# Performance work log

Measured on AMD Instinct MI355X. Metric: run time of the kernel, lower is better.

## Reference

```python
import jax, jax.numpy as jnp
import numpy as np

IN_DIM = 768
ATT_DIM = 512
N_HEADS = 8
HEAD_DIM = ATT_DIM // N_HEADS


def setup_inputs() -> dict:
    key = jax.random.key(0)
    k1, k2, k3 = jax.random.split(key, 3)
    X = jax.random.normal(k1, (4, 2048, IN_DIM), dtype=jnp.float32)
    # qkv linear (no bias): weight [3*att_dim, in_dim], torch convention y = x W^T
    W_qkv = jax.random.normal(k2, (3 * ATT_DIM, IN_DIM), dtype=jnp.float32) * (1.0 / np.sqrt(IN_DIM))
    W_out = jax.random.normal(k3, (IN_DIM, ATT_DIM), dtype=jnp.float32) * (1.0 / np.sqrt(ATT_DIM))
    b_out = jnp.zeros((IN_DIM,), dtype=jnp.float32)
    return {"X": X, "W_qkv": W_qkv, "W_out": W_out, "b_out": b_out}


def reference(X, W_qkv, W_out, b_out):
    b, n, _ = X.shape
    QKV = jnp.einsum('bnf,cf->bnc', X, W_qkv)  # [b, n, 3*att_dim]
    # rearrange 'b n (p h d) -> p b h n d'
    QKV = QKV.reshape(b, n, 3, N_HEADS, HEAD_DIM).transpose(2, 0, 3, 1, 4)
    Q, K, V = QKV[0], QKV[1], QKV[2]  # each [b, h, n, d]
    scores = jnp.einsum('bhid,bhjd->bhij', Q, K) / np.sqrt(HEAD_DIM)
    A = jax.nn.softmax(scores, axis=-1)  # dropout p=0 -> identity
    Y = jnp.einsum('bhij,bhjd->bhid', A, V)
    Y = Y.transpose(0, 2, 1, 3).reshape(b, n, ATT_DIM)  # 'b h n d -> b n (h d)'
    return jnp.einsum('bna,oa->bno', Y, W_out) + b_out
```

## Files before the change

### kernel.cpp

```cpp
#include <hip/hip_runtime.h>

typedef __bf16 bf16;
typedef unsigned int u32;
typedef __attribute__((ext_vector_type(8))) __bf16 bf16x8;
typedef __attribute__((ext_vector_type(4))) __bf16 bf16x4;
typedef __attribute__((ext_vector_type(4))) float floatx4;
typedef __attribute__((ext_vector_type(16))) float floatx16;
typedef __attribute__((ext_vector_type(4))) int int4v;

#define IN_DIM  768
#define ATT_DIM 512
#define NH      8
#define HD      64
#define BATCH   4
#define SEQ     2048
#define M_TOT   (BATCH*SEQ)
#define QKV_N   (3*ATT_DIM)

#define QSCALE 0.18033688011112042f

__device__ __forceinline__ void cp16(void* lds, const void* g) {
    __builtin_amdgcn_global_load_lds((const __attribute__((address_space(1))) u32*)g,
                                     (__attribute__((address_space(3))) u32*)lds, 16, 0, 0);
}
__device__ __forceinline__ const bf16* swz(const bf16* b, int row, int chunk) {
    return b + row * 64 + (((chunk) ^ (row & 7)) << 3);
}
__device__ __forceinline__ const bf16* swz128(const bf16* b, int row, int chunk) {
    return b + row * 128 + (((chunk) ^ (row & 15)) << 3);
}

__device__ __forceinline__ int cvtpk_bf16(float lo, float hi) {
    int r;
    asm("v_cvt_pk_bf16_f32 %0, %1, %2" : "=v"(r) : "v"(lo), "v"(hi));
    return r;
}
__device__ __forceinline__ void plswap(int& a, int& b) {
    asm("v_permlane32_swap_b32 %0, %1" : "+v"(a), "+v"(b));
}

#define N8_X  (M_TOT * IN_DIM / 8)
#define N8_WQ (QKV_N * IN_DIM / 8)
#define N8_WO (IN_DIM * ATT_DIM / 8)
#define N8_ALL (N8_X + N8_WQ + N8_WO)

__global__ __launch_bounds__(256) void cvt_all(const float* __restrict__ X,
                                               const float* __restrict__ Wq,
                                               const float* __restrict__ Wo,
                                               bf16* __restrict__ Xb,
                                               bf16* __restrict__ Wqb,
                                               bf16* __restrict__ Wob) {
    int i = blockIdx.x * 256 + threadIdx.x;
    const float* s; bf16* d; int off;
    if (i < N8_X)            { s = X;  d = Xb;  off = i; }
    else if (i < N8_X+N8_WQ) { s = Wq; d = Wqb; off = i - N8_X; }
    else                     { s = Wo; d = Wob; off = i - N8_X - N8_WQ; }
    const float4 a = ((const float4*)s)[2*off];
    const float4 b = ((const float4*)s)[2*off+1];
    bf16x8 o = {(bf16)a.x,(bf16)a.y,(bf16)a.z,(bf16)a.w,
                (bf16)b.x,(bf16)b.y,(bf16)b.z,(bf16)b.w};
    ((bf16x8*)d)[off] = o;
}

__global__ __launch_bounds__(256) void qkv_gemm(const bf16* __restrict__ Xb,
                                                const bf16* __restrict__ Wb,
                                                bf16* __restrict__ Q,
                                                bf16* __restrict__ Kv,
                                                bf16* __restrict__ VT) {
    __shared__ __align__(16) char smraw[34816];
    bf16* As = (bf16*)smraw;
    bf16* Bs = (bf16*)(smraw + 16384);

    const int tid  = threadIdx.x;
    const int bm0  = blockIdx.y * 128;
    const int bn0  = blockIdx.x * 128;
    const int wave = tid >> 6, lane = tid & 63;
    const int quad = lane >> 4, l15 = lane & 15;
    const int wm = (wave >> 1) * 64, wn = (wave & 1) * 64;
    const int r8 = lane >> 3, cc = (lane & 7) ^ r8;

    const bf16* ag = Xb + (size_t)(bm0 + wave * 32 + r8) * IN_DIM + cc * 8;
    const bf16* bg = Wb + (size_t)(bn0 + wave * 32 + r8) * IN_DIM + cc * 8;

    floatx4 acc[4][4];
#pragma unroll
    for (int i = 0; i < 4; ++i)
#pragma unroll
        for (int j = 0; j < 4; ++j) acc[i][j] = (floatx4){0.f, 0.f, 0.f, 0.f};

    for (int kt = 0; kt < IN_DIM / 64; ++kt) {
        __syncthreads();
#pragma unroll
        for (int it = 0; it < 4; ++it) {
            cp16(&As[(wave * 32 + it * 8) * 64], ag + it * (8 * IN_DIM) + kt * 64);
            cp16(&Bs[(wave * 32 + it * 8) * 64], bg + it * (8 * IN_DIM) + kt * 64);
        }
        __syncthreads();

        bf16x8 af[2][4], bfr[2][4];
#pragma unroll
        for (int kh = 0; kh < 2; ++kh)
#pragma unroll
            for (int i = 0; i < 4; ++i) {
                af[kh][i]  = *(const bf16x8*)swz(As, wm + i * 16 + l15, kh * 4 + quad);
                bfr[kh][i] = *(const bf16x8*)swz(Bs, wn + i * 16 + l15, kh * 4 + quad);
            }
#pragma unroll
        for (int kh = 0; kh < 2; ++kh)
#pragma unroll
            for (int i = 0; i < 4; ++i)
#pragma unroll
                for (int j = 0; j < 4; ++j)
                    acc[i][j] = __builtin_amdgcn_mfma_f32_16x16x32_bf16(af[kh][i], bfr[kh][j], acc[i][j], 0, 0, 0);
    }

    const int b = bm0 >> 11, nbase = bm0 & 2047;

    if (bn0 < 1024) {
#pragma unroll
        for (int i = 0; i < 4; ++i)
#pragma unroll
            for (int j = 0; j < 4; ++j)
#pragma unroll
                for (int r = 0; r < 4; ++r) {
                    const int row = bm0 + wm + i * 16 + quad * 4 + r;
                    const int col = bn0 + wn + j * 16 + l15;
                    const float v = acc[i][j][r];
                    const int rem = col & 511;
                    const int h = rem >> 6, d = rem & 63;
                    const int n = row & 2047;
                    const size_t idx = (((size_t)((row >> 11) * NH + h)) * SEQ + n) * HD + d;
                    if (col < 512) Q[idx]  = (bf16)(v * QSCALE);
                    else           Kv[idx] = (bf16)v;
                }
    } else {
        __syncthreads();
        bf16 (*Ts)[136] = (bf16(*)[136])smraw;
#pragma unroll
        for (int i = 0; i < 4; ++i)
#pragma unroll
            for (int j = 0; j < 4; ++j) {
                bf16x4 pk = {(bf16)acc[i][j][0], (bf16)acc[i][j][1],
                             (bf16)acc[i][j][2], (bf16)acc[i][j][3]};
                *(bf16x4*)&Ts[wn + j * 16 + l15][wm + i * 16 + quad * 4] = pk;
            }
        __syncthreads();
        const int cb = bn0 - 1024;
#pragma unroll
        for (int t2 = 0; t2 < 8; ++t2) {
            const int id = tid + t2 * 256;
            const int c = id >> 4, nc = (id & 15) * 8;
            const int col = cb + c;
            const int h = col >> 6, d = col & 63;
            *(bf16x8*)&VT[(((size_t)(b * NH + h)) * HD + d) * SEQ + nbase + nc] =
                *(const bf16x8*)&Ts[c][nc];
        }
    }
}

__global__ __launch_bounds__(256, 4) void attn(const bf16* __restrict__ Q,
                                               const bf16* __restrict__ K,
                                               const bf16* __restrict__ VT,
                                               bf16* __restrict__ Y) {
    __shared__ bf16 Ks[2][64 * 64];
    __shared__ bf16 VTs[2][64 * 64];

    const int tid  = threadIdx.x;
    const int wave = tid >> 6, lane = tid & 63;
    const int l31  = lane & 31, hi = lane >> 5;
    const int bh = blockIdx.x;
    const int q0 = blockIdx.y * 128;
    const bf16* Qg = Q  + (size_t)bh * SEQ * HD;
    const bf16* Kg = K  + (size_t)bh * SEQ * HD;
    const bf16* Vg = VT + (size_t)bh * HD * SEQ;

    bf16x8 aq[4];
    {
        const bf16* qrow = Qg + (size_t)(q0 + wave * 32 + l31) * HD;
#pragma unroll
        for (int c = 0; c < 4; ++c)
            aq[c] = *(const bf16x8*)(qrow + c * 16 + hi * 8);
    }

    const int r8 = lane >> 3, cc8 = (lane & 7) ^ r8;
    const bf16* kgw = Kg + (size_t)(wave * 16 + r8) * HD + cc8 * 8;
    const bf16* vgw = Vg + (size_t)(wave * 16 + r8) * SEQ + cc8 * 8;

    float l = 0.f;
    floatx16 o[2];
#pragma unroll
    for (int i = 0; i < 16; ++i) { o[0][i] = 0.f; o[1][i] = 0.f; }

#pragma unroll
    for (int it = 0; it < 2; ++it) {
        cp16(&Ks[0][(wave * 16 + it * 8) * 64], kgw + (size_t)(it * 8) * HD);
        cp16(&VTs[0][(wave * 16 + it * 8) * 64], vgw + (size_t)(it * 8) * SEQ);
    }

    for (int kt = 0; kt < SEQ / 64; ++kt) {
        const int cur = kt & 1;
        __syncthreads();
        if (kt < SEQ / 64 - 1) {
#pragma unroll
            for (int it = 0; it < 2; ++it) {
                cp16(&Ks[cur ^ 1][(wave * 16 + it * 8) * 64],
                     kgw + (size_t)((kt + 1) * 64 + it * 8) * HD);
                cp16(&VTs[cur ^ 1][(wave * 16 + it * 8) * 64],
                     vgw + (size_t)(it * 8) * SEQ + (kt + 1) * 64);
            }
        }

#pragma unroll
        for (int kb = 0; kb < 2; ++kb) {
            const int krow = kb * 32 + l31;
            floatx16 s;
#pragma unroll
            for (int i = 0; i < 16; ++i) s[i] = 0.f;
#pragma unroll
            for (int c = 0; c < 4; ++c) {
                const bf16x8 kf = *(const bf16x8*)swz(Ks[cur], krow, c * 2 + hi);
                s = __builtin_amdgcn_mfma_f32_32x32x16_bf16(kf, aq[c], s, 0, 0, 0);
            }
            float p[16];
#pragma unroll
            for (int i = 0; i < 16; ++i) p[i] = __builtin_amdgcn_exp2f(s[i]);
            {
                const float t0 = (p[0] + p[1]) + (p[2] + p[3]);
                const float t1 = (p[4] + p[5]) + (p[6] + p[7]);
                const float t2 = (p[8] + p[9]) + (p[10] + p[11]);
                const float t3 = (p[12] + p[13]) + (p[14] + p[15]);
                l += (t0 + t1) + (t2 + t3);
            }
            int w[8];
#pragma unroll
            for (int i = 0; i < 8; ++i) w[i] = cvtpk_bf16(p[2 * i], p[2 * i + 1]);
            plswap(w[0], w[2]); plswap(w[1], w[3]);
            plswap(w[4], w[6]); plswap(w[5], w[7]);
            const int4v f0i = {w[0], w[1], w[2], w[3]};
            const int4v f1i = {w[4], w[5], w[6], w[7]};
            const bf16x8 f0 = __builtin_bit_cast(bf16x8, f0i);
            const bf16x8 f1 = __builtin_bit_cast(bf16x8, f1i);
#pragma unroll
            for (int db = 0; db < 2; ++db) {
                const int vrow = db * 32 + l31;
                const bf16x8 v0 = *(const bf16x8*)swz(VTs[cur], vrow, kb * 4 + hi);
                const bf16x8 v1 = *(const bf16x8*)swz(VTs[cur], vrow, kb * 4 + 2 + hi);
                o[db] = __builtin_amdgcn_mfma_f32_32x32x16_bf16(f0, v0, o[db], 0, 0, 0);
                o[db] = __builtin_amdgcn_mfma_f32_32x32x16_bf16(f1, v1, o[db], 0, 0, 0);
            }
        }
    }

    l += __shfl_xor(l, 32, 64);
    const float inv = 1.0f / l;
    const int b = bh >> 3, h = bh & 7;
#pragma unroll
    for (int reg = 0; reg < 16; ++reg) {
        const int qr = (reg & 3) + 8 * (reg >> 2) + 4 * hi;
        const float li = __int_as_float(
            __builtin_amdgcn_ds_bpermute(qr << 2, __float_as_int(inv)));
        const int n = q0 + wave * 32 + qr;
        bf16* yrow = Y + ((size_t)(b * SEQ + n)) * ATT_DIM + h * HD + l31;
        yrow[0]  = (bf16)(o[0][reg] * li);
        yrow[32] = (bf16)(o[1][reg] * li);
    }
}

__global__ __launch_bounds__(256) void out_gemm(const bf16* __restrict__ Yb,
                                                const bf16* __restrict__ Wb,
                                                const float* __restrict__ bias,
                                                float* __restrict__ out) {
    __shared__ __align__(16) bf16 As[128 * 64];
    __shared__ __align__(16) bf16 Bs[128 * 64];

    const int tid  = threadIdx.x;
    const int bm0  = blockIdx.y * 128;
    const int bn0  = blockIdx.x * 128;
    const int wave = tid >> 6, lane = tid & 63;
    const int quad = lane >> 4, l15 = lane & 15;
    const int wm = (wave >> 1) * 64, wn = (wave & 1) * 64;
    const int r8 = lane >> 3, cc = (lane & 7) ^ r8;

    const bf16* ag = Yb + (size_t)(bm0 + wave * 32 + r8) * ATT_DIM + cc * 8;
    const bf16* bg = Wb + (size_t)(bn0 + wave * 32 + r8) * ATT_DIM + cc * 8;

    floatx4 acc[4][4];
#pragma unroll
    for (int i = 0; i < 4; ++i)
#pragma unroll
        for (int j = 0; j < 4; ++j) acc[i][j] = (floatx4){0.f, 0.f, 0.f, 0.f};

    for (int kt = 0; kt < ATT_DIM / 64; ++kt) {
        __syncthreads();
#pragma unroll
        for (int it = 0; it < 4; ++it) {
            cp16(&As[(wave * 32 + it * 8) * 64], ag + it * (8 * ATT_DIM) + kt * 64);
            cp16(&Bs[(wave * 32 + it * 8) * 64], bg + it * (8 * ATT_DIM) + kt * 64);
        }
        __syncthreads();

        bf16x8 af[2][4], bfr[2][4];
#pragma unroll
        for (int kh = 0; kh < 2; ++kh)
#pragma unroll
            for (int i = 0; i < 4; ++i) {
                af[kh][i]  = *(const bf16x8*)swz(As, wm + i * 16 + l15, kh * 4 + quad);
                bfr[kh][i] = *(const bf16x8*)swz(Bs, wn + i * 16 + l15, kh * 4 + quad);
            }
#pragma unroll
        for (int kh = 0; kh < 2; ++kh)
#pragma unroll
            for (int i = 0; i < 4; ++i)
#pragma unroll
                for (int j = 0; j < 4; ++j)
                    acc[i][j] = __builtin_amdgcn_mfma_f32_16x16x32_bf16(af[kh][i], bfr[kh][j], acc[i][j], 0, 0, 0);
    }

#pragma unroll
    for (int i = 0; i < 4; ++i)
#pragma unroll
        for (int j = 0; j < 4; ++j)
#pragma unroll
            for (int r = 0; r < 4; ++r) {
                const int row = bm0 + wm + i * 16 + quad * 4 + r;
                const int col = bn0 + wn + j * 16 + l15;
                out[(size_t)row * IN_DIM + col] = acc[i][j][r] + bias[col];
            }
}

extern "C" void kernel_launch(void* const* d_in, const int* in_sizes, int n_in,
                              void* d_out, int out_size, void* d_ws, size_t ws_size,
                              hipStream_t stream) {
    const float* X    = (const float*)d_in[0];
    const float* Wqkv = (const float*)d_in[1];
    const float* Wout = (const float*)d_in[2];
    const float* bout = (const float*)d_in[3];
    float* out = (float*)d_out;

    char* ws = (char*)d_ws;
    size_t off = 0;
    bf16* Xb  = (bf16*)(ws + off); off += (size_t)M_TOT * IN_DIM * 2;
    bf16* Wqb = (bf16*)(ws + off); off += (size_t)QKV_N * IN_DIM * 2;
    bf16* Wob = (bf16*)(ws + off); off += (size_t)IN_DIM * ATT_DIM * 2;
    const size_t T = (size_t)BATCH * NH * SEQ * HD * 2;
    bf16* Q  = (bf16*)(ws + off); off += T;
    bf16* K  = (bf16*)(ws + off); off += T;
    bf16* VT = (bf16*)(ws + off); off += T;
    bf16* Y  = (bf16*)(ws + off); off += T;

    cvt_all<<<N8_ALL / 256, 256, 0, stream>>>(X, Wqkv, Wout, Xb, Wqb, Wob);
    qkv_gemm<<<dim3(QKV_N / 128, M_TOT / 128), 256, 0, stream>>>(Xb, Wqb, Q, K, VT);
    attn<<<dim3(BATCH * NH, SEQ / 128), 256, 0, stream>>>(Q, K, VT, Y);
    out_gemm<<<dim3(IN_DIM / 128, M_TOT / 128), 256, 0, stream>>>(Y, Wob, bout, out);
}
```

Before: 162.7 us.

## Process two query groups per wave in attention and pre-permute K/VT for split LDS reads

Each attention wave now handles 64 query rows (two 32-row groups) instead of 32, so one set of K and V fragments read from LDS feeds twice as many MFMAs. Blocks shrink to 128 threads with launch_bounds(128,1). The QKV GEMM epilogue also stores K and VT with 8-byte halves swapped on alternating rows, and the attention kernel reads them back as two 8-byte LDS loads in swapped order, presumably to avoid bank conflicts. The cost is doubled accumulator register pressure and fewer waves per block, and the occupancy hint of 1 may limit latency hiding.

```diff
diff --git a/kernel.cpp b/kernel.cpp
--- a/kernel.cpp
+++ b/kernel.cpp
@@ -26,8 +26,12 @@
 __device__ __forceinline__ const bf16* swz(const bf16* b, int row, int chunk) {
     return b + row * 64 + (((chunk) ^ (row & 7)) << 3);
 }
-__device__ __forceinline__ const bf16* swz128(const bf16* b, int row, int chunk) {
-    return b + row * 128 + (((chunk) ^ (row & 15)) << 3);
+__device__ __forceinline__ bf16x8 ld_swz8(const bf16* tile, int row, int chunk) {
+    const char* base = (const char*)(tile + row * 64) + (((chunk ^ (row & 7)) << 4));
+    const int off = row & 8;
+    const bf16x4 h0 = *(const bf16x4*)(base + off);
+    const bf16x4 h1 = *(const bf16x4*)(base + (off ^ 8));
+    return (bf16x8){h0[0], h0[1], h0[2], h0[3], h1[0], h1[1], h1[2], h1[3]};
 }
 
 __device__ __forceinline__ int cvtpk_bf16(float lo, float hi) {
@@ -130,8 +134,8 @@
                     const int h = rem >> 6, d = rem & 63;
                     const int n = row & 2047;
                     const size_t idx = (((size_t)((row >> 11) * NH + h)) * SEQ + n) * HD + d;
-                    if (col < 512) Q[idx]  = (bf16)(v * QSCALE);
-                    else           Kv[idx] = (bf16)v;
+                    if (col < 512) Q[idx] = (bf16)(v * QSCALE);
+                    else           Kv[idx ^ (size_t)((n >> 1) & 4)] = (bf16)v;
                 }
     } else {
         __syncthreads();
@@ -152,13 +156,15 @@
             const int c = id >> 4, nc = (id & 15) * 8;
             const int col = cb + c;
             const int h = col >> 6, d = col & 63;
-            *(bf16x8*)&VT[(((size_t)(b * NH + h)) * HD + d) * SEQ + nbase + nc] =
-                *(const bf16x8*)&Ts[c][nc];
-        }
-    }
-}
-
-__global__ __launch_bounds__(256, 4) void attn(const bf16* __restrict__ Q,
+            bf16x8 val = *(const bf16x8*)&Ts[c][nc];
+            if (d & 8)
+                val = __builtin_shufflevector(val, val, 4, 5, 6, 7, 0, 1, 2, 3);
+            *(bf16x8*)&VT[(((size_t)(b * NH + h)) * HD + d) * SEQ + nbase + nc] = val;
+        }
+    }
+}
+
+__global__ __launch_bounds__(128, 1) void attn(const bf16* __restrict__ Q,
                                                const bf16* __restrict__ K,
                                                const bf16* __restrict__ VT,
                                                bf16* __restrict__ Y) {
@@ -174,27 +180,30 @@
     const bf16* Kg = K  + (size_t)bh * SEQ * HD;
     const bf16* Vg = VT + (size_t)bh * HD * SEQ;
 
-    bf16x8 aq[4];
-    {
-        const bf16* qrow = Qg + (size_t)(q0 + wave * 32 + l31) * HD;
+    bf16x8 aq[2][4];
+#pragma unroll
+    for (int g = 0; g < 2; ++g) {
+        const bf16* qrow = Qg + (size_t)(q0 + wave * 64 + g * 32 + l31) * HD;
 #pragma unroll
         for (int c = 0; c < 4; ++c)
-            aq[c] = *(const bf16x8*)(qrow + c * 16 + hi * 8);
+            aq[g][c] = *(const bf16x8*)(qrow + c * 16 + hi * 8);
     }
 
     const int r8 = lane >> 3, cc8 = (lane & 7) ^ r8;
-    const bf16* kgw = Kg + (size_t)(wave * 16 + r8) * HD + cc8 * 8;
-    const bf16* vgw = Vg + (size_t)(wave * 16 + r8) * SEQ + cc8 * 8;
-
-    float l = 0.f;
-    floatx16 o[2];
-#pragma unroll
-    for (int i = 0; i < 16; ++i) { o[0][i] = 0.f; o[1][i] = 0.f; }
-
-#pragma unroll
-    for (int it = 0; it < 2; ++it) {
-        cp16(&Ks[0][(wave * 16 + it * 8) * 64], kgw + (size_t)(it * 8) * HD);
-        cp16(&VTs[0][(wave * 16 + it * 8) * 64], vgw + (size_t)(it * 8) * SEQ);
+    const bf16* kgw = Kg + (size_t)(wave * 32 + r8) * HD + cc8 * 8;
+    const bf16* vgw = Vg + (size_t)(wave * 32 + r8) * SEQ + cc8 * 8;
+
+    float l[2] = {0.f, 0.f};
+    floatx16 o[2][2];
+#pragma unroll
+    for (int g = 0; g < 2; ++g)
+#pragma unroll
+        for (int i = 0; i < 16; ++i) { o[g][0][i] = 0.f; o[g][1][i] = 0.f; }
+
+#pragma unroll
+    for (int it = 0; it < 4; ++it) {
+        cp16(&Ks[0][(wave * 32 + it * 8) * 64], kgw + (size_t)(it * 8) * HD);
+        cp16(&VTs[0][(wave * 32 + it * 8) * 64], vgw + (size_t)(it * 8) * SEQ);
     }
 
     for (int kt = 0; kt < SEQ / 64; ++kt) {
@@ -202,10 +211,10 @@
         __syncthreads();
         if (kt < SEQ / 64 - 1) {
 #pragma unroll
-            for (int it = 0; it < 2; ++it) {
-                cp16(&Ks[cur ^ 1][(wave * 16 + it * 8) * 64],
+            for (int it = 0; it < 4; ++it) {
+                cp16(&Ks[cur ^ 1][(wave * 32 + it * 8) * 64],
                      kgw + (size_t)((kt + 1) * 64 + it * 8) * HD);
-                cp16(&VTs[cur ^ 1][(wave * 16 + it * 8) * 64],
+                cp16(&VTs[cur ^ 1][(wave * 32 + it * 8) * 64],
                      vgw + (size_t)(it * 8) * SEQ + (kt + 1) * 64);
             }
         }
@@ -213,56 +222,68 @@
 #pragma unroll
         for (int kb = 0; kb < 2; ++kb) {
             const int krow = kb * 32 + l31;
-            floatx16 s;
-#pragma unroll
-            for (int i = 0; i < 16; ++i) s[i] = 0.f;
-#pragma unroll
-            for (int c = 0; c < 4; ++c) {
-                const bf16x8 kf = *(const bf16x8*)swz(Ks[cur], krow, c * 2 + hi);
-                s = __builtin_amdgcn_mfma_f32_32x32x16_bf16(kf, aq[c], s, 0, 0, 0);
-            }
-            float p[16];
-#pragma unroll
-            for (int i = 0; i < 16; ++i) p[i] = __builtin_amdgcn_exp2f(s[i]);
-            {
-                const float t0 = (p[0] + p[1]) + (p[2] + p[3]);
-                const float t1 = (p[4] + p[5]) + (p[6] + p[7]);
-                const float t2 = (p[8] + p[9]) + (p[10] + p[11]);
-                const float t3 = (p[12] + p[13]) + (p[14] + p[15]);
-                l += (t0 + t1) + (t2 + t3);
-            }
-            int w[8];
-#pragma unroll
-            for (int i = 0; i < 8; ++i) w[i] = cvtpk_bf16(p[2 * i], p[2 * i + 1]);
-            plswap(w[0], w[2]); plswap(w[1], w[3]);
-            plswap(w[4], w[6]); plswap(w[5], w[7]);
-            const int4v f0i = {w[0], w[1], w[2], w[3]};
-            const int4v f1i = {w[4], w[5], w[6], w[7]};
-            const bf16x8 f0 = __builtin_bit_cast(bf16x8, f0i);
-            const bf16x8 f1 = __builtin_bit_cast(bf16x8, f1i);
+            bf16x8 kf[4];
+#pragma unroll
+            for (int c = 0; c < 4; ++c)
+                kf[c] = ld_swz8(Ks[cur], krow, c * 2 + hi);
+            bf16x8 vf[2][2];
 #pragma unroll
             for (int db = 0; db < 2; ++db) {
-                const int vrow = db * 32 + l31;
-                const bf16x8 v0 = *(const bf16x8*)swz(VTs[cur], vrow, kb * 4 + hi);
-                const bf16x8 v1 = *(const bf16x8*)swz(VTs[cur], vrow, kb * 4 + 2 + hi);
-                o[db] = __builtin_amdgcn_mfma_f32_32x32x16_bf16(f0, v0, o[db], 0, 0, 0);
-                o[db] = __builtin_amdgcn_mfma_f32_32x32x16_bf16(f1, v1, o[db], 0, 0, 0);
-            }
-        }
-    }
-
-    l += __shfl_xor(l, 32, 64);
-    const float inv = 1.0f / l;
+                vf[db][0] = ld_swz8(VTs[cur], db * 32 + l31, kb * 4 + hi);
+                vf[db][1] = ld_swz8(VTs[cur], db * 32 + l31, kb * 4 + 2 + hi);
+            }
+#pragma unroll
+            for (int g = 0; g < 2; ++g) {
+                floatx16 s;
+#pragma unroll
+                for (int i = 0; i < 16; ++i) s[i] = 0.f;
+#pragma unroll
+                for (int c = 0; c < 4; ++c)
+                    s = __builtin_amdgcn_mfma_f32_32x32x16_bf16(kf[c], aq[g][c], s, 0, 0, 0);
+                float p[16];
+#pragma unroll
+                for (int i = 0; i < 16; ++i) p[i] = __builtin_amdgcn_exp2f(s[i]);
+                {
+                    const float t0 = (p[0] + p[1]) + (p[2] + p[3]);
+                    const float t1 = (p[4] + p[5]) + (p[6] + p[7]);
+                    const float t2 = (p[8] + p[9]) + (p[10] + p[11]);
+                    const float t3 = (p[12] + p[13]) + (p[14] + p[15]);
+                    l[g] += (t0 + t1) + (t2 + t3);
+                }
+                int w[8];
+#pragma unroll
+                for (int i = 0; i < 8; ++i) w[i] = cvtpk_bf16(p[2 * i], p[2 * i + 1]);
+                plswap(w[0], w[2]); plswap(w[1], w[3]);
+                plswap(w[4], w[6]); plswap(w[5], w[7]);
+                const int4v f0i = {w[0], w[1], w[2], w[3]};
+                const int4v f1i = {w[4], w[5], w[6], w[7]};
+                const bf16x8 f0 = __builtin_bit_cast(bf16x8, f0i);
+                const bf16x8 f1 = __builtin_bit_cast(bf16x8, f1i);
+#pragma unroll
+                for (int db = 0; db < 2; ++db) {
+                    o[g][db] = __builtin_amdgcn_mfma_f32_32x32x16_bf16(f0, vf[db][0], o[g][db], 0, 0, 0);
+                    o[g][db] = __builtin_amdgcn_mfma_f32_32x32x16_bf16(f1, vf[db][1], o[g][db], 0, 0, 0);
+                }
+            }
+        }
+    }
+
     const int b = bh >> 3, h = bh & 7;
 #pragma unroll
-    for (int reg = 0; reg < 16; ++reg) {
-        const int qr = (reg & 3) + 8 * (reg >> 2) + 4 * hi;
-        const float li = __int_as_float(
-            __builtin_amdgcn_ds_bpermute(qr << 2, __float_as_int(inv)));
-        const int n = q0 + wave * 32 + qr;
-        bf16* yrow = Y + ((size_t)(b * SEQ + n)) * ATT_DIM + h * HD + l31;
-        yrow[0]  = (bf16)(o[0][reg] * li);
-        yrow[32] = (bf16)(o[1][reg] * li);
+    for (int g = 0; g < 2; ++g) {
+        float lg = l[g];
+        lg += __shfl_xor(lg, 32, 64);
+        const float inv = 1.0f / lg;
+#pragma unroll
+        for (int reg = 0; reg < 16; ++reg) {
+            const int qr = (reg & 3) + 8 * (reg >> 2) + 4 * hi;
+            const float li = __int_as_float(
+                __builtin_amdgcn_ds_bpermute(qr << 2, __float_as_int(inv)));
+            const int n = q0 + wave * 64 + g * 32 + qr;
+            bf16* yrow = Y + ((size_t)(b * SEQ + n)) * ATT_DIM + h * HD + l31;
+            yrow[0]  = (bf16)(o[g][0][reg] * li);
+            yrow[32] = (bf16)(o[g][1][reg] * li);
+        }
     }
 }
 
@@ -350,6 +371,6 @@
 
     cvt_all<<<N8_ALL / 256, 256, 0, stream>>>(X, Wqkv, Wout, Xb, Wqb, Wob);
     qkv_gemm<<<dim3(QKV_N / 128, M_TOT / 128), 256, 0, stream>>>(Xb, Wqb, Q, K, VT);
-    attn<<<dim3(BATCH * NH, SEQ / 128), 256, 0, stream>>>(Q, K, VT, Y);
+    attn<<<dim3(BATCH * NH, SEQ / 128), 128, 0, stream>>>(Q, K, VT, Y);
     out_gemm<<<dim3(IN_DIM / 128, M_TOT / 128), 256, 0, stream>>>(Y, Wob, bout, out);
 }
```

Result: slower. 181.9 us (+11.8%).

## Split attention over key range with combine kernel and conflict-free LDS layout

Applied to the files above, without the earlier changes.

Splits the attention kernel's key loop into two halves along a new grid dimension. This doubles the number of blocks (512 → 1024) to improve occupancy across the GPU's CUs, and partial fp32 outputs and row sums are merged in a new combine kernel. It also permutes the K and VT layouts written by the QKV GEMM so LDS fragment reads become two 8-byte loads meant to avoid bank conflicts. It hoists the fragment loads ahead of the MFMAs and raises wave priority around the MFMA sections. The cost is an extra kernel launch and a round trip of fp32 partials through global memory. Correctness relies on softmax not subtracting the max, which lets the partial sums be added directly.

```diff
diff --git a/kernel.cpp b/kernel.cpp
--- a/kernel.cpp
+++ b/kernel.cpp
@@ -26,8 +26,12 @@
 __device__ __forceinline__ const bf16* swz(const bf16* b, int row, int chunk) {
     return b + row * 64 + (((chunk) ^ (row & 7)) << 3);
 }
-__device__ __forceinline__ const bf16* swz128(const bf16* b, int row, int chunk) {
-    return b + row * 128 + (((chunk) ^ (row & 15)) << 3);
+__device__ __forceinline__ bf16x8 ld_swz8(const bf16* tile, int row, int chunk) {
+    const char* base = (const char*)(tile + row * 64) + (((chunk ^ (row & 7)) << 4));
+    const int off = row & 8;
+    const bf16x4 h0 = *(const bf16x4*)(base + off);
+    const bf16x4 h1 = *(const bf16x4*)(base + (off ^ 8));
+    return (bf16x8){h0[0], h0[1], h0[2], h0[3], h1[0], h1[1], h1[2], h1[3]};
 }
 
 __device__ __forceinline__ int cvtpk_bf16(float lo, float hi) {
@@ -130,8 +134,8 @@
                     const int h = rem >> 6, d = rem & 63;
                     const int n = row & 2047;
                     const size_t idx = (((size_t)((row >> 11) * NH + h)) * SEQ + n) * HD + d;
-                    if (col < 512) Q[idx]  = (bf16)(v * QSCALE);
-                    else           Kv[idx] = (bf16)v;
+                    if (col < 512) Q[idx] = (bf16)(v * QSCALE);
+                    else           Kv[idx ^ (size_t)((n >> 1) & 4)] = (bf16)v;
                 }
     } else {
         __syncthreads();
@@ -152,8 +156,10 @@
             const int c = id >> 4, nc = (id & 15) * 8;
             const int col = cb + c;
             const int h = col >> 6, d = col & 63;
-            *(bf16x8*)&VT[(((size_t)(b * NH + h)) * HD + d) * SEQ + nbase + nc] =
-                *(const bf16x8*)&Ts[c][nc];
+            bf16x8 val = *(const bf16x8*)&Ts[c][nc];
+            if (d & 8)
+                val = __builtin_shufflevector(val, val, 4, 5, 6, 7, 0, 1, 2, 3);
+            *(bf16x8*)&VT[(((size_t)(b * NH + h)) * HD + d) * SEQ + nbase + nc] = val;
         }
     }
 }
@@ -161,7 +167,8 @@
 __global__ __launch_bounds__(256, 4) void attn(const bf16* __restrict__ Q,
                                                const bf16* __restrict__ K,
                                                const bf16* __restrict__ VT,
-                                               bf16* __restrict__ Y) {
+                                               float* __restrict__ Of,
+                                               float* __restrict__ Lf) {
     __shared__ bf16 Ks[2][64 * 64];
     __shared__ bf16 VTs[2][64 * 64];
 
@@ -170,6 +177,8 @@
     const int l31  = lane & 31, hi = lane >> 5;
     const int bh = blockIdx.x;
     const int q0 = blockIdx.y * 128;
+    const int ks = blockIdx.z;
+    const int kt0 = ks * (SEQ / 128);
     const bf16* Qg = Q  + (size_t)bh * SEQ * HD;
     const bf16* Kg = K  + (size_t)bh * SEQ * HD;
     const bf16* Vg = VT + (size_t)bh * HD * SEQ;
@@ -193,14 +202,16 @@
 
 #pragma unroll
     for (int it = 0; it < 2; ++it) {
-        cp16(&Ks[0][(wave * 16 + it * 8) * 64], kgw + (size_t)(it * 8) * HD);
-        cp16(&VTs[0][(wave * 16 + it * 8) * 64], vgw + (size_t)(it * 8) * SEQ);
-    }
-
-    for (int kt = 0; kt < SEQ / 64; ++kt) {
+        cp16(&Ks[0][(wave * 16 + it * 8) * 64],
+             kgw + (size_t)(kt0 * 64 + it * 8) * HD);
+        cp16(&VTs[0][(wave * 16 + it * 8) * 64],
+             vgw + (size_t)(it * 8) * SEQ + kt0 * 64);
+    }
+
+    for (int kt = kt0; kt < kt0 + SEQ / 128; ++kt) {
         const int cur = kt & 1;
         __syncthreads();
-        if (kt < SEQ / 64 - 1) {
+        if (kt < kt0 + SEQ / 128 - 1) {
 #pragma unroll
             for (int it = 0; it < 2; ++it) {
                 cp16(&Ks[cur ^ 1][(wave * 16 + it * 8) * 64],
@@ -213,14 +224,25 @@
 #pragma unroll
         for (int kb = 0; kb < 2; ++kb) {
             const int krow = kb * 32 + l31;
+            bf16x8 kf[4];
+#pragma unroll
+            for (int c = 0; c < 4; ++c)
+                kf[c] = ld_swz8(Ks[cur], krow, c * 2 + hi);
+            bf16x8 vf[2][2];
+#pragma unroll
+            for (int db = 0; db < 2; ++db) {
+                vf[db][0] = ld_swz8(VTs[cur], db * 32 + l31, kb * 4 + hi);
+                vf[db][1] = ld_swz8(VTs[cur], db * 32 + l31, kb * 4 + 2 + hi);
+            }
+
             floatx16 s;
 #pragma unroll
             for (int i = 0; i < 16; ++i) s[i] = 0.f;
-#pragma unroll
-            for (int c = 0; c < 4; ++c) {
-                const bf16x8 kf = *(const bf16x8*)swz(Ks[cur], krow, c * 2 + hi);
-                s = __builtin_amdgcn_mfma_f32_32x32x16_bf16(kf, aq[c], s, 0, 0, 0);
-            }
+            __builtin_amdgcn_s_setprio(1);
+#pragma unroll
+            for (int c = 0; c < 4; ++c)
+                s = __builtin_amdgcn_mfma_f32_32x32x16_bf16(kf[c], aq[c], s, 0, 0, 0);
+            __builtin_amdgcn_s_setprio(0);
             float p[16];
 #pragma unroll
             for (int i = 0; i < 16; ++i) p[i] = __builtin_amdgcn_exp2f(s[i]);
@@ -240,30 +262,48 @@
             const int4v f1i = {w[4], w[5], w[6], w[7]};
             const bf16x8 f0 = __builtin_bit_cast(bf16x8, f0i);
             const bf16x8 f1 = __builtin_bit_cast(bf16x8, f1i);
+            __builtin_amdgcn_s_setprio(1);
 #pragma unroll
             for (int db = 0; db < 2; ++db) {
-                const int vrow = db * 32 + l31;
-                const bf16x8 v0 = *(const bf16x8*)swz(VTs[cur], vrow, kb * 4 + hi);
-                const bf16x8 v1 = *(const bf16x8*)swz(VTs[cur], vrow, kb * 4 + 2 + hi);
-                o[db] = __builtin_amdgcn_mfma_f32_32x32x16_bf16(f0, v0, o[db], 0, 0, 0);
-                o[db] = __builtin_amdgcn_mfma_f32_32x32x16_bf16(f1, v1, o[db], 0, 0, 0);
-            }
+                o[db] = __builtin_amdgcn_mfma_f32_32x32x16_bf16(f0, vf[db][0], o[db], 0, 0, 0);
+                o[db] = __builtin_amdgcn_mfma_f32_32x32x16_bf16(f1, vf[db][1], o[db], 0, 0, 0);
+            }
+            __builtin_amdgcn_s_setprio(0);
         }
     }
 
     l += __shfl_xor(l, 32, 64);
-    const float inv = 1.0f / l;
-    const int b = bh >> 3, h = bh & 7;
+    if (hi == 0)
+        Lf[((size_t)ks * 32 + bh) * SEQ + q0 + wave * 32 + l31] = l;
 #pragma unroll
     for (int reg = 0; reg < 16; ++reg) {
         const int qr = (reg & 3) + 8 * (reg >> 2) + 4 * hi;
-        const float li = __int_as_float(
-            __builtin_amdgcn_ds_bpermute(qr << 2, __float_as_int(inv)));
         const int n = q0 + wave * 32 + qr;
-        bf16* yrow = Y + ((size_t)(b * SEQ + n)) * ATT_DIM + h * HD + l31;
-        yrow[0]  = (bf16)(o[0][reg] * li);
-        yrow[32] = (bf16)(o[1][reg] * li);
-    }
+        float* op = Of + (((size_t)ks * 32 + bh) * SEQ + n) * HD + l31;
+        op[0]  = o[0][reg];
+        op[32] = o[1][reg];
+    }
+}
+
+__global__ __launch_bounds__(256) void attn_combine(const float* __restrict__ Of,
+                                                    const float* __restrict__ Lf,
+                                                    bf16* __restrict__ Y) {
+    const int i  = blockIdx.x * 256 + threadIdx.x;
+    const int d0 = (i & 7) * 8;
+    const int q  = (i >> 3) & 2047;
+    const int bh = i >> 14;
+    const float inv = 1.0f / (Lf[(size_t)bh * SEQ + q] +
+                              Lf[(size_t)(32 + bh) * SEQ + q]);
+    const float4 a0 = *(const float4*)&Of[(((size_t)bh * SEQ) + q) * HD + d0];
+    const float4 a1 = *(const float4*)&Of[(((size_t)bh * SEQ) + q) * HD + d0 + 4];
+    const float4 b0 = *(const float4*)&Of[(((size_t)(32 + bh) * SEQ) + q) * HD + d0];
+    const float4 b1 = *(const float4*)&Of[(((size_t)(32 + bh) * SEQ) + q) * HD + d0 + 4];
+    bf16x8 r = {(bf16)((a0.x + b0.x) * inv), (bf16)((a0.y + b0.y) * inv),
+                (bf16)((a0.z + b0.z) * inv), (bf16)((a0.w + b0.w) * inv),
+                (bf16)((a1.x + b1.x) * inv), (bf16)((a1.y + b1.y) * inv),
+                (bf16)((a1.z + b1.z) * inv), (bf16)((a1.w + b1.w) * inv)};
+    const int b = bh >> 3, h = bh & 7;
+    *(bf16x8*)&Y[((size_t)(b * SEQ + q)) * ATT_DIM + h * HD + d0] = r;
 }
 
 __global__ __launch_bounds__(256) void out_gemm(const bf16* __restrict__ Yb,
@@ -347,9 +387,12 @@
     bf16* K  = (bf16*)(ws + off); off += T;
     bf16* VT = (bf16*)(ws + off); off += T;
     bf16* Y  = (bf16*)(ws + off); off += T;
+    float* Of = (float*)(ws + off); off += (size_t)2 * 32 * SEQ * HD * 4;
+    float* Lf = (float*)(ws + off); off += (size_t)2 * 32 * SEQ * 4;
 
     cvt_all<<<N8_ALL / 256, 256, 0, stream>>>(X, Wqkv, Wout, Xb, Wqb, Wob);
     qkv_gemm<<<dim3(QKV_N / 128, M_TOT / 128), 256, 0, stream>>>(Xb, Wqb, Q, K, VT);
-    attn<<<dim3(BATCH * NH, SEQ / 128), 256, 0, stream>>>(Q, K, VT, Y);
+    attn<<<dim3(BATCH * NH, SEQ / 128, 2), 256, 0, stream>>>(Q, K, VT, Of, Lf);
+    attn_combine<<<(32 * SEQ * 8) / 256, 256, 0, stream>>>(Of, Lf, Y);
     out_gemm<<<dim3(IN_DIM / 128, M_TOT / 128), 256, 0, stream>>>(Y, Wob, bout, out);
 }
```

Measured after the change: 199.2 us. 22.5% more time.

## Split attention MFMA accumulators, hoist LDS loads, add setprio and half-swizzled K/V layout

Applied to the files above, without the earlier changes.

The attention inner loop now loads all K and V fragments up front, splits the QK^T and PV MFMA chains into two independent accumulators each so consecutive MFMAs do not depend on one another, and raises wave priority around the MFMA blocks. The QKV GEMM epilogue writes K and V^T with the two 8-byte halves of each 16-byte chunk swapped on alternating row groups, and the attention kernel reads them back as two bf16x4 loads to undo the swap, apparently to spread LDS bank accesses. Launch bounds drop from 4 to 2 blocks per SM to leave room for the extra accumulator registers. The risks are lower occupancy and twice as many LDS read instructions.

```diff
diff --git a/kernel.cpp b/kernel.cpp
--- a/kernel.cpp
+++ b/kernel.cpp
@@ -26,8 +26,12 @@
 __device__ __forceinline__ const bf16* swz(const bf16* b, int row, int chunk) {
     return b + row * 64 + (((chunk) ^ (row & 7)) << 3);
 }
-__device__ __forceinline__ const bf16* swz128(const bf16* b, int row, int chunk) {
-    return b + row * 128 + (((chunk) ^ (row & 15)) << 3);
+__device__ __forceinline__ bf16x8 ld_swz8(const bf16* tile, int row, int chunk) {
+    const char* base = (const char*)(tile + row * 64) + (((chunk ^ (row & 7)) << 4));
+    const int off = row & 8;
+    const bf16x4 h0 = *(const bf16x4*)(base + off);
+    const bf16x4 h1 = *(const bf16x4*)(base + (off ^ 8));
+    return (bf16x8){h0[0], h0[1], h0[2], h0[3], h1[0], h1[1], h1[2], h1[3]};
 }
 
 __device__ __forceinline__ int cvtpk_bf16(float lo, float hi) {
@@ -116,7 +120,7 @@
 
     const int b = bm0 >> 11, nbase = bm0 & 2047;
 
-    if (bn0 < 1024) {
+    if (bn0 < 512) {
 #pragma unroll
         for (int i = 0; i < 4; ++i)
 #pragma unroll
@@ -125,13 +129,24 @@
                 for (int r = 0; r < 4; ++r) {
                     const int row = bm0 + wm + i * 16 + quad * 4 + r;
                     const int col = bn0 + wn + j * 16 + l15;
-                    const float v = acc[i][j][r];
-                    const int rem = col & 511;
-                    const int h = rem >> 6, d = rem & 63;
+                    const int h = col >> 6, d = col & 63;
                     const int n = row & 2047;
                     const size_t idx = (((size_t)((row >> 11) * NH + h)) * SEQ + n) * HD + d;
-                    if (col < 512) Q[idx]  = (bf16)(v * QSCALE);
-                    else           Kv[idx] = (bf16)v;
+                    Q[idx] = (bf16)(acc[i][j][r] * QSCALE);
+                }
+    } else if (bn0 < 1024) {
+#pragma unroll
+        for (int i = 0; i < 4; ++i)
+#pragma unroll
+            for (int j = 0; j < 4; ++j)
+#pragma unroll
+                for (int r = 0; r < 4; ++r) {
+                    const int row = bm0 + wm + i * 16 + quad * 4 + r;
+                    const int col = bn0 - 512 + wn + j * 16 + l15;
+                    const int h = col >> 6, d = col & 63;
+                    const int n = row & 2047;
+                    const size_t idx = (((size_t)((row >> 11) * NH + h)) * SEQ + n) * HD + d;
+                    Kv[idx ^ (size_t)((n >> 1) & 4)] = (bf16)acc[i][j][r];
                 }
     } else {
         __syncthreads();
@@ -152,13 +167,15 @@
             const int c = id >> 4, nc = (id & 15) * 8;
             const int col = cb + c;
             const int h = col >> 6, d = col & 63;
-            *(bf16x8*)&VT[(((size_t)(b * NH + h)) * HD + d) * SEQ + nbase + nc] =
-                *(const bf16x8*)&Ts[c][nc];
-        }
-    }
-}
-
-__global__ __launch_bounds__(256, 4) void attn(const bf16* __restrict__ Q,
+            bf16x8 val = *(const bf16x8*)&Ts[c][nc];
+            if (d & 8)
+                val = __builtin_shufflevector(val, val, 4, 5, 6, 7, 0, 1, 2, 3);
+            *(bf16x8*)&VT[(((size_t)(b * NH + h)) * HD + d) * SEQ + nbase + nc] = val;
+        }
+    }
+}
+
+__global__ __launch_bounds__(256, 2) void attn(const bf16* __restrict__ Q,
                                                const bf16* __restrict__ K,
                                                const bf16* __restrict__ VT,
                                                bf16* __restrict__ Y) {
@@ -187,9 +204,12 @@
     const bf16* vgw = Vg + (size_t)(wave * 16 + r8) * SEQ + cc8 * 8;
 
     float l = 0.f;
-    floatx16 o[2];
-#pragma unroll
-    for (int i = 0; i < 16; ++i) { o[0][i] = 0.f; o[1][i] = 0.f; }
+    floatx16 oa[2], ob[2];
+#pragma unroll
+    for (int i = 0; i < 16; ++i) {
+        oa[0][i] = 0.f; oa[1][i] = 0.f;
+        ob[0][i] = 0.f; ob[1][i] = 0.f;
+    }
 
 #pragma unroll
     for (int it = 0; it < 2; ++it) {
@@ -213,17 +233,30 @@
 #pragma unroll
         for (int kb = 0; kb < 2; ++kb) {
             const int krow = kb * 32 + l31;
-            floatx16 s;
-#pragma unroll
-            for (int i = 0; i < 16; ++i) s[i] = 0.f;
-#pragma unroll
-            for (int c = 0; c < 4; ++c) {
-                const bf16x8 kf = *(const bf16x8*)swz(Ks[cur], krow, c * 2 + hi);
-                s = __builtin_amdgcn_mfma_f32_32x32x16_bf16(kf, aq[c], s, 0, 0, 0);
-            }
+            bf16x8 kf[4];
+#pragma unroll
+            for (int c = 0; c < 4; ++c)
+                kf[c] = ld_swz8(Ks[cur], krow, c * 2 + hi);
+            bf16x8 vf[2][2];
+#pragma unroll
+            for (int db = 0; db < 2; ++db) {
+                vf[db][0] = ld_swz8(VTs[cur], db * 32 + l31, kb * 4 + hi);
+                vf[db][1] = ld_swz8(VTs[cur], db * 32 + l31, kb * 4 + 2 + hi);
+            }
+
+            floatx16 s0, s1;
+#pragma unroll
+            for (int i = 0; i < 16; ++i) { s0[i] = 0.f; s1[i] = 0.f; }
+            __builtin_amdgcn_s_setprio(1);
+            s0 = __builtin_amdgcn_mfma_f32_32x32x16_bf16(kf[0], aq[0], s0, 0, 0, 0);
+            s1 = __builtin_amdgcn_mfma_f32_32x32x16_bf16(kf[1], aq[1], s1, 0, 0, 0);
+            s0 = __builtin_amdgcn_mfma_f32_32x32x16_bf16(kf[2], aq[2], s0, 0, 0, 0);
+            s1 = __builtin_amdgcn_mfma_f32_32x32x16_bf16(kf[3], aq[3], s1, 0, 0, 0);
+            __builtin_amdgcn_s_setprio(0);
             float p[16];
 #pragma unroll
-            for (int i = 0; i < 16; ++i) p[i] = __builtin_amdgcn_exp2f(s[i]);
+            for (int i = 0; i < 16; ++i)
+                p[i] = __builtin_amdgcn_exp2f(s0[i] + s1[i]);
             {
                 const float t0 = (p[0] + p[1]) + (p[2] + p[3]);
                 const float t1 = (p[4] + p[5]) + (p[6] + p[7]);
@@ -240,14 +273,13 @@
             const int4v f1i = {w[4], w[5], w[6], w[7]};
             const bf16x8 f0 = __builtin_bit_cast(bf16x8, f0i);
             const bf16x8 f1 = __builtin_bit_cast(bf16x8, f1i);
+            __builtin_amdgcn_s_setprio(1);
 #pragma unroll
             for (int db = 0; db < 2; ++db) {
-                const int vrow = db * 32 + l31;
-                const bf16x8 v0 = *(const bf16x8*)swz(VTs[cur], vrow, kb * 4 + hi);
-                const bf16x8 v1 = *(const bf16x8*)swz(VTs[cur], vrow, kb * 4 + 2 + hi);
-                o[db] = __builtin_amdgcn_mfma_f32_32x32x16_bf16(f0, v0, o[db], 0, 0, 0);
-                o[db] = __builtin_amdgcn_mfma_f32_32x32x16_bf16(f1, v1, o[db], 0, 0, 0);
-            }
+                oa[db] = __builtin_amdgcn_mfma_f32_32x32x16_bf16(f0, vf[db][0], oa[db], 0, 0, 0);
+                ob[db] = __builtin_amdgcn_mfma_f32_32x32x16_bf16(f1, vf[db][1], ob[db], 0, 0, 0);
+            }
+            __builtin_amdgcn_s_setprio(0);
         }
     }
 
@@ -261,8 +293,8 @@
             __builtin_amdgcn_ds_bpermute(qr << 2, __float_as_int(inv)));
         const int n = q0 + wave * 32 + qr;
         bf16* yrow = Y + ((size_t)(b * SEQ + n)) * ATT_DIM + h * HD + l31;
-        yrow[0]  = (bf16)(o[0][reg] * li);
-        yrow[32] = (bf16)(o[1][reg] * li);
+        yrow[0]  = (bf16)((oa[0][reg] + ob[0][reg]) * li);
+        yrow[32] = (bf16)((oa[1][reg] + ob[1][reg]) * li);
     }
 }
 
```

Result: slower. 175.0 us (+7.6%).
